# Kernel tuning notes

Hardware: AMD Instinct MI355X
Metric: run time of the kernel (lower is better)

## Reference

```python
import jax, jax.numpy as jnp
import numpy as np

# RRFU config (matches init_kwargs)
S = 2          # scale_factor
G = 4          # groups
K = 3          # sample_k
C = 64         # in_channels
B, H, W_IN = 4, 128, 128
SC = S * S     # s_c
KC = K * K     # sample_c (3x3 = 9)


def setup_inputs() -> dict:
    key = jax.random.key(0)
    ks = jax.random.split(key, 9)
    x = jax.random.normal(ks[0], (B, C, H, W_IN), jnp.float32)
    # 1x1 conv weights stored as (out_ch, in_ch); std chosen per module's init
    # (mask convs are zero-init in the original; use small random so math is nontrivial)
    w_off = jax.random.normal(ks[1], (G * SC * 2, C), jnp.float32) * 0.001
    b_off = jnp.zeros((G * SC * 2,), jnp.float32)
    w_offm = jax.random.normal(ks[2], (G * SC * 2, C), jnp.float32) * 0.01
    b_offm = jnp.zeros((G * SC * 2,), jnp.float32)
    w_sk = jax.random.normal(ks[3], (KC, C), jnp.float32) * 0.005
    b_sk = jnp.zeros((KC,), jnp.float32)
    w_km = jax.random.normal(ks[4], (KC, C), jnp.float32) * 0.01
    b_km = jnp.zeros((KC,), jnp.float32)
    return {"x": x, "w_off": w_off, "b_off": b_off, "w_offm": w_offm,
            "b_offm": b_offm, "w_sk": w_sk, "b_sk": b_sk, "w_km": w_km, "b_km": b_km}


def _conv1x1(x, w, b):
    return jnp.einsum('oc,bchw->bohw', w, x) + b[None, :, None, None]


def _bilinear_border(img, iy, ix):
    """img: (Cg,H,W); iy,ix: (Ho,Wo) pixel coords. grid_sample bilinear, padding_mode='border'."""
    Hh, Ww = img.shape[1], img.shape[2]
    ix = jnp.clip(ix, 0.0, Ww - 1.0)
    iy = jnp.clip(iy, 0.0, Hh - 1.0)
    x0 = jnp.floor(ix)
    y0 = jnp.floor(iy)
    wx = ix - x0
    wy = iy - y0
    x0i = x0.astype(jnp.int32)
    y0i = y0.astype(jnp.int32)
    x1i = jnp.minimum(x0i + 1, Ww - 1)
    y1i = jnp.minimum(y0i + 1, Hh - 1)
    v00 = img[:, y0i, x0i]
    v01 = img[:, y0i, x1i]
    v10 = img[:, y1i, x0i]
    v11 = img[:, y1i, x1i]
    return (v00 * (1 - wx) * (1 - wy) + v01 * wx * (1 - wy)
            + v10 * (1 - wx) * wy + v11 * wx * wy)


def reference(x, w_off, b_off, w_offm, b_offm, w_sk, b_sk, w_km, b_km):
    b0, c0, h0, w0 = x.shape
    # learned offsets, gated by sigmoid mask
    off = _conv1x1(x, w_off, b_off) * jax.nn.sigmoid(_conv1x1(x, w_offm, b_offm))
    bg = b0 * G
    # (b, g*S*S*2, h, w) -> (bg, S, S, 2, h, w) -> (bg, h, S, w, S, 2) -> (bg, S*h, S*w, 2)
    off = off.reshape(bg, S, S, 2, h0, w0).transpose(0, 4, 1, 5, 2, 3).reshape(bg, S * h0, S * w0, 2)
    Ho, Wo = S * h0, S * w0
    # coord_base + offset, normalized then un-normalized for align_corners=False grid_sample
    cx = jnp.arange(Wo, dtype=x.dtype) + 0.5
    cy = jnp.arange(Ho, dtype=x.dtype) + 0.5
    ix = (cx[None, None, :] + off[..., 0]) * (w0 / Wo) - 0.5  # (bg, Ho, Wo)
    iy = (cy[None, :, None] + off[..., 1]) * (h0 / Ho) - 0.5
    x_r = x.reshape(bg, c0 // G, h0, w0)
    x_def = jax.vmap(_bilinear_border)(x_r, iy, ix).reshape(b0, c0, Ho, Wo)
    # CARAFE-style dynamic reassembly: softmax kernel over 3x3 neighborhood
    sk = _conv1x1(x_def, w_sk, b_sk) * jax.nn.sigmoid(_conv1x1(x_def, w_km, b_km))
    skn = jax.nn.softmax(sk, axis=1)  # (b, 9, Ho, Wo)
    pad = K // 2
    xp = jnp.pad(x_def, ((0, 0), (0, 0), (pad, pad), (pad, pad)))  # zero pad like F.unfold
    out = jnp.zeros_like(x_def)
    for ky in range(K):  # fixed 3x3 taps; avoids materializing (b,c,9,Ho,Wo)
        for kx in range(K):
            out = out + skn[:, ky * K + kx][:, None] * xp[:, :, ky:ky + Ho, kx:kx + Wo]
    return out
```

## Files before the change

### kernel.cpp

```cpp
#include <hip/hip_runtime.h>
#include <hip/hip_fp16.h>

typedef _Float16 h2 __attribute__((ext_vector_type(2)));

constexpr int Bc  = 4;
constexpr int Cc  = 64;
constexpr int H0  = 128;
constexpr int W0  = 128;
constexpr int HW  = H0 * W0;
constexpr int Gc  = 4;
constexpr int HOc = H0 * 2;
constexpr int WOc = W0 * 2;

constexpr int TW = 16;
constexpr int TH = 8;
constexpr int HX = TW + 2;
constexpr int HY = TH + 2;
constexpr int NHALO = HX * HY;
constexpr int NTASK = Gc * NHALO;

constexpr int SXC = 10;
constexpr int SYC = 6;
constexpr int SN  = SXC * SYC;
constexpr int NPAIR = Cc / 2;

__device__ __forceinline__ float dot2(h2 a, unsigned bw, float c) {
    union { unsigned u; h2 h; } cv; cv.u = bw;
#if __has_builtin(__builtin_amdgcn_fdot2)
    return __builtin_amdgcn_fdot2(a, cv.h, c, false);
#else
    return fmaf((float)a[0], (float)cv.h[0],
                fmaf((float)a[1], (float)cv.h[1], c));
#endif
}

__global__ __launch_bounds__(256) void kT_prep(
    const float* __restrict__ w_off, const float* __restrict__ w_offm,
    const float* __restrict__ w_sk,  const float* __restrict__ w_km,
    float* __restrict__ wT, __half2* __restrict__ wpk)
{
    const int i = blockIdx.x * 256 + threadIdx.x;
    if (i < 4096) {
        const int mat = i >> 11;
        const int rem = i & 2047;
        const int c   = rem >> 5;
        const int r   = rem & 31;
        wT[i] = (mat ? w_offm : w_off)[r * Cc + c];
    } else if (i < 4096 + 576) {
        const int j   = i - 4096;
        const int mat = j >= 288;
        const int jj  = mat ? j - 288 : j;
        const int k   = jj >> 5;
        const int c2  = jj & 31;
        const float* src = mat ? w_km : w_sk;
        wpk[j] = __floats2half2_rn(src[k * Cc + 2 * c2],
                                   src[k * Cc + 2 * c2 + 1]);
    }
}

__global__ __launch_bounds__(256) void k0_offsets(
    const float* __restrict__ x, const float* __restrict__ wT,
    const float* __restrict__ b_off, const float* __restrict__ b_offm,
    __half2* __restrict__ offbuf)
{
    const int b    = blockIdx.y;
    const int t    = threadIdx.x;
    const int wave = t >> 6, lane = t & 63;
    const int r0   = __builtin_amdgcn_readfirstlane((wave & 1) * 16);
    const int px   = blockIdx.x * 128 + (wave >> 1) * 64 + lane;

    float a[16], m[16];
#pragma unroll
    for (int q = 0; q < 16; ++q) { a[q] = 0.f; m[q] = 0.f; }

    const float* xp  = x + (size_t)b * Cc * HW + px;
    const float* w0p = wT + r0;
    const float* w1p = wT + 2048 + r0;

#pragma unroll 2
    for (int c = 0; c < Cc; ++c) {
        const float xv = xp[c * HW];
#pragma unroll
        for (int q = 0; q < 16; ++q) {
            a[q] = fmaf(w0p[c * 32 + q], xv, a[q]);
            m[q] = fmaf(w1p[c * 32 + q], xv, m[q]);
        }
    }

#pragma unroll
    for (int j = 0; j < 8; ++j) {
        const int r = r0 + 2 * j;
        const float sx = 1.f / (1.f + __expf(-(m[2 * j]     + b_offm[r])));
        const float sy = 1.f / (1.f + __expf(-(m[2 * j + 1] + b_offm[r + 1])));
        const float vx = (a[2 * j]     + b_off[r])     * sx;
        const float vy = (a[2 * j + 1] + b_off[r + 1]) * sy;
        offbuf[((size_t)b * 16 + (r >> 1)) * HW + px] = __floats2half2_rn(vx, vy);
    }
}

__global__ __launch_bounds__(256) void k1_fused(
    const float* __restrict__ x, const __half2* __restrict__ offbuf,
    const unsigned* __restrict__ wsku, const float* __restrict__ b_sk,
    const float* __restrict__ b_km,
    float* __restrict__ out)
{
    __shared__ h2    xd2[NPAIR][NHALO];
    __shared__ float ovl[2304];
    h2*       xstage2 = (h2*)ovl;
    float*    kmb     = ovl;
    unsigned* sknb    = (unsigned*)(ovl + 128 * 9);

    const unsigned* wkmu = wsku + 288;

    const int b    = blockIdx.y;
    const int tile = blockIdx.x;
    const int ox = (tile & 15) * TW;
    const int oy = (tile >> 4) * TH;
    const int t  = threadIdx.x;
    const int syr = (oy >> 1) - 1;
    const int sxr = (ox >> 1) - 1;

    const float* xb = x + (size_t)b * Cc * HW;

    for (int i = t; i < NPAIR * SN; i += 256) {
        const int c2  = i / SN;
        const int rem = i - c2 * SN;
        const int r   = rem / SXC;
        const int j   = rem - r * SXC;
        const int yy  = min(max(syr + r, 0), H0 - 1);
        const int xx  = min(max(sxr + j, 0), W0 - 1);
        const float f0 = xb[(size_t)(2 * c2)     * HW + yy * W0 + xx];
        const float f1 = xb[(size_t)(2 * c2 + 1) * HW + yy * W0 + xx];
        xstage2[i] = h2{(_Float16)f0, (_Float16)f1};
    }
    __syncthreads();

    for (int task = t; task < NTASK; task += 256) {
        const int g   = task / NHALO;
        const int pix = task - g * NHALO;
        const int hy  = pix / HX;
        const int hx  = pix - hy * HX;
        const int gy  = oy - 1 + hy;
        const int gx  = ox - 1 + hx;
        if (gy < 0 || gy >= HOc || gx < 0 || gx >= WOc) {
#pragma unroll
            for (int p = 0; p < 8; ++p) xd2[g * 8 + p][pix] = (h2)0;
            continue;
        }
        const int sy = gy & 1, sx = gx & 1;
        const int h  = gy >> 1, w  = gx >> 1;
        const __half2 o2 = offbuf[((size_t)b * 16 + g * 4 + sy * 2 + sx) * HW
                                  + h * W0 + w];
        const float offx = __low2float(o2);
        const float offy = __high2float(o2);

        float ix = ((float)gx + 0.5f + offx) * 0.5f - 0.5f;
        float iy = ((float)gy + 0.5f + offy) * 0.5f - 0.5f;
        ix = fminf(fmaxf(ix, 0.f), (float)(W0 - 1));
        iy = fminf(fmaxf(iy, 0.f), (float)(H0 - 1));
        const float x0f = floorf(ix), y0f = floorf(iy);
        const float wx = ix - x0f,   wy = iy - y0f;
        const int x0 = (int)x0f, y0 = (int)y0f;
        const int x1 = min(x0 + 1, W0 - 1), y1 = min(y0 + 1, H0 - 1);
        const float w00 = (1.f - wx) * (1.f - wy);
        const float w01 = wx * (1.f - wy);
        const float w10 = (1.f - wx) * wy;
        const float w11 = wx * wy;

        const int j0 = x0 - sxr, j1 = x1 - sxr;
        const int i0 = y0 - syr, i1 = y1 - syr;
        const bool inl = (j0 >= 0) & (j1 < SXC) & (i0 >= 0) & (i1 < SYC);

        if (inl) {
            const int o00 = i0 * SXC + j0, o01 = i0 * SXC + j1;
            const int o10 = i1 * SXC + j0, o11 = i1 * SXC + j1;
            const _Float16 W00 = (_Float16)w00, W01 = (_Float16)w01;
            const _Float16 W10 = (_Float16)w10, W11 = (_Float16)w11;
            const h2* s2 = xstage2 + (g * 8) * SN;
#pragma unroll
            for (int p = 0; p < 8; ++p) {
                const h2* pc = s2 + p * SN;
                xd2[g * 8 + p][pix] =
                    pc[o00] * W00 + pc[o01] * W01 + pc[o10] * W10 + pc[o11] * W11;
            }
        } else {
            const int o00 = y0 * W0 + x0, o01 = y0 * W0 + x1;
            const int o10 = y1 * W0 + x0, o11 = y1 * W0 + x1;
#pragma unroll
            for (int p = 0; p < 8; ++p) {
                const float* pc0 = xb + (size_t)(g * 16 + 2 * p) * HW;
                const float* pc1 = pc0 + HW;
                const float v0 = w00 * pc0[o00] + w01 * pc0[o01]
                               + w10 * pc0[o10] + w11 * pc0[o11];
                const float v1 = w00 * pc1[o00] + w01 * pc1[o01]
                               + w10 * pc1[o10] + w11 * pc1[o11];
                xd2[g * 8 + p][pix] = h2{(_Float16)v0, (_Float16)v1};
            }
        }
    }
    __syncthreads();

    {
        const int p   = t & 127;
        const int ctr = ((p >> 4) + 1) * HX + (p & 15) + 1;
        h2 xv[NPAIR];
#pragma unroll
        for (int c2 = 0; c2 < NPAIR; ++c2) xv[c2] = xd2[c2][ctr];

        float acc[9];
        if (t < 128) {
#pragma unroll
            for (int k = 0; k < 9; ++k) {
                float a = 0.f;
#pragma unroll
                for (int c2 = 0; c2 < NPAIR; ++c2)
                    a = dot2(xv[c2], wsku[k * 32 + c2], a);
                acc[k] = a;
            }
        } else {
#pragma unroll
            for (int k = 0; k < 9; ++k) {
                float a = 0.f;
#pragma unroll
                for (int c2 = 0; c2 < NPAIR; ++c2)
                    a = dot2(xv[c2], wkmu[k * 32 + c2], a);
                kmb[p * 9 + k] = a;
            }
        }
        __syncthreads();

        if (t < 128) {
            float sv[9], mx = -1e30f;
#pragma unroll
            for (int k = 0; k < 9; ++k) {
                const float z = kmb[p * 9 + k] + b_km[k];
                sv[k] = (acc[k] + b_sk[k]) / (1.f + __expf(-z));
                mx = fmaxf(mx, sv[k]);
            }
            float sum = 0.f;
#pragma unroll
            for (int k = 0; k < 9; ++k) { sv[k] = __expf(sv[k] - mx); sum += sv[k]; }
            const float inv = 1.f / sum;
#pragma unroll
            for (int k = 0; k < 9; ++k) {
                const unsigned hu = __half_as_ushort(__float2half(sv[k] * inv));
                sknb[p * 9 + k] = hu | (hu << 16);
            }
        }
    }
    __syncthreads();

    {
        const int sq    = t & 31;
        const int chunk = t >> 5;
        const int sqx = sq & 7, sqy = sq >> 3;
        const int hx0 = 2 * sqx, hy0 = 2 * sqy;
        const int p00 = (2 * sqy) * TW + 2 * sqx;

        union { unsigned u; h2 h; } s00[9], s01[9], s10[9], s11[9];
#pragma unroll
        for (int k = 0; k < 9; ++k) {
            s00[k].u = sknb[p00 * 9 + k];        s01[k].u = sknb[(p00 + 1) * 9 + k];
            s10[k].u = sknb[(p00 + TW) * 9 + k]; s11[k].u = sknb[(p00 + TW + 1) * 9 + k];
        }
        const int orow0 = oy + 2 * sqy, ocol0 = ox + 2 * sqx;

#pragma unroll
        for (int i = 0; i < 4; ++i) {
            const int pr = chunk * 4 + i;
            h2 wd[4][4];
#pragma unroll
            for (int ry = 0; ry < 4; ++ry) {
                const int base = (hy0 + ry) * HX + hx0;
#pragma unroll
                for (int rx = 0; rx < 4; ++rx)
                    wd[ry][rx] = xd2[pr][base + rx];
            }
            h2 a00 = (h2)0, a01 = (h2)0, a10 = (h2)0, a11 = (h2)0;
#pragma unroll
            for (int ky = 0; ky < 3; ++ky)
#pragma unroll
                for (int kx = 0; kx < 3; ++kx) {
                    const int k = ky * 3 + kx;
                    a00 += s00[k].h * wd[ky    ][kx    ];
                    a01 += s01[k].h * wd[ky    ][kx + 1];
                    a10 += s10[k].h * wd[ky + 1][kx    ];
                    a11 += s11[k].h * wd[ky + 1][kx + 1];
                }
            float* ob0 = out + ((size_t)(b * Cc + 2 * pr)) * (HOc * WOc)
                             + (size_t)orow0 * WOc + ocol0;
            float* ob1 = ob0 + (size_t)(HOc * WOc);
            *reinterpret_cast<float2*>(ob0)       = make_float2((float)a00[0], (float)a01[0]);
            *reinterpret_cast<float2*>(ob0 + WOc) = make_float2((float)a10[0], (float)a11[0]);
            *reinterpret_cast<float2*>(ob1)       = make_float2((float)a00[1], (float)a01[1]);
            *reinterpret_cast<float2*>(ob1 + WOc) = make_float2((float)a10[1], (float)a11[1]);
        }
    }
}

extern "C" void kernel_launch(void* const* d_in, const int* in_sizes, int n_in,
                              void* d_out, int out_size, void* d_ws, size_t ws_size,
                              hipStream_t stream)
{
    const float* x      = (const float*)d_in[0];
    const float* w_off  = (const float*)d_in[1];
    const float* b_off  = (const float*)d_in[2];
    const float* w_offm = (const float*)d_in[3];
    const float* b_offm = (const float*)d_in[4];
    const float* w_sk   = (const float*)d_in[5];
    const float* b_sk   = (const float*)d_in[6];
    const float* w_km   = (const float*)d_in[7];
    const float* b_km   = (const float*)d_in[8];
    float* outp = (float*)d_out;

    const size_t off_bytes = (size_t)Bc * 16 * HW * sizeof(__half2);
    const size_t wt_bytes  = 4096 * sizeof(float);
    const size_t pk_bytes  = 576 * sizeof(__half2);
    if (ws_size < off_bytes + wt_bytes + pk_bytes) return;
    __half2* offbuf = (__half2*)d_ws;
    float*   wT     = (float*)((char*)d_ws + off_bytes);
    __half2* wpk    = (__half2*)((char*)d_ws + off_bytes + wt_bytes);

    dim3 blk(256);
    hipLaunchKernelGGL(kT_prep, dim3(19), blk, 0, stream,
                       w_off, w_offm, w_sk, w_km, wT, wpk);

    dim3 g0(HW / 128, Bc);
    hipLaunchKernelGGL(k0_offsets, g0, blk, 0, stream,
                       x, wT, b_off, b_offm, offbuf);

    dim3 g1(512, Bc);
    hipLaunchKernelGGL(k1_fused, g1, blk, 0, stream,
                       x, offbuf, (const unsigned*)wpk, b_sk, b_km, outp);
}
```

Before: 68.26 us.

## Emit channel-last fp16 copy of x and pixel-major offsets for fused kernel

```diff
diff --git a/kernel.cpp b/kernel.cpp
--- a/kernel.cpp
+++ b/kernel.cpp
@@ -24,8 +24,10 @@
 constexpr int SN  = SXC * SYC;
 constexpr int NPAIR = Cc / 2;
 
+union hu32 { unsigned u; h2 h; };
+
 __device__ __forceinline__ float dot2(h2 a, unsigned bw, float c) {
-    union { unsigned u; h2 h; } cv; cv.u = bw;
+    hu32 cv; cv.u = bw;
 #if __has_builtin(__builtin_amdgcn_fdot2)
     return __builtin_amdgcn_fdot2(a, cv.h, c, false);
 #else
@@ -37,17 +39,19 @@
 __global__ __launch_bounds__(256) void kT_prep(
     const float* __restrict__ w_off, const float* __restrict__ w_offm,
     const float* __restrict__ w_sk,  const float* __restrict__ w_km,
-    float* __restrict__ wT, __half2* __restrict__ wpk)
+    __half2* __restrict__ wpk0, __half2* __restrict__ wpk)
 {
     const int i = blockIdx.x * 256 + threadIdx.x;
-    if (i < 4096) {
-        const int mat = i >> 11;
-        const int rem = i & 2047;
-        const int c   = rem >> 5;
+    if (i < 2048) {
+        const int c2  = i >> 6;
+        const int rem = i & 63;
+        const int mat = rem >> 5;
         const int r   = rem & 31;
-        wT[i] = (mat ? w_offm : w_off)[r * Cc + c];
-    } else if (i < 4096 + 576) {
-        const int j   = i - 4096;
+        const float* src = mat ? w_offm : w_off;
+        wpk0[i] = __floats2half2_rn(src[r * Cc + 2 * c2],
+                                    src[r * Cc + 2 * c2 + 1]);
+    } else if (i < 2048 + 576) {
+        const int j   = i - 2048;
         const int mat = j >= 288;
         const int jj  = mat ? j - 288 : j;
         const int k   = jj >> 5;
@@ -59,47 +63,57 @@
 }
 
 __global__ __launch_bounds__(256) void k0_offsets(
-    const float* __restrict__ x, const float* __restrict__ wT,
+    const float* __restrict__ x, const unsigned* __restrict__ wpk0,
     const float* __restrict__ b_off, const float* __restrict__ b_offm,
-    __half2* __restrict__ offbuf)
+    __half2* __restrict__ offbuf, unsigned* __restrict__ xt)
 {
     const int b    = blockIdx.y;
     const int t    = threadIdx.x;
     const int wave = t >> 6, lane = t & 63;
-    const int r0   = __builtin_amdgcn_readfirstlane((wave & 1) * 16);
-    const int px   = blockIdx.x * 128 + (wave >> 1) * 64 + lane;
-
-    float a[16], m[16];
-#pragma unroll
-    for (int q = 0; q < 16; ++q) { a[q] = 0.f; m[q] = 0.f; }
-
-    const float* xp  = x + (size_t)b * Cc * HW + px;
-    const float* w0p = wT + r0;
-    const float* w1p = wT + 2048 + r0;
-
-#pragma unroll 2
-    for (int c = 0; c < Cc; ++c) {
-        const float xv = xp[c * HW];
-#pragma unroll
-        for (int q = 0; q < 16; ++q) {
-            a[q] = fmaf(w0p[c * 32 + q], xv, a[q]);
-            m[q] = fmaf(w1p[c * 32 + q], xv, m[q]);
-        }
-    }
-
-#pragma unroll
-    for (int j = 0; j < 8; ++j) {
+    const int r0   = __builtin_amdgcn_readfirstlane(wave * 8);
+    const int px   = blockIdx.x * 64 + lane;
+
+    float a[8], m[8];
+#pragma unroll
+    for (int q = 0; q < 8; ++q) { a[q] = 0.f; m[q] = 0.f; }
+    unsigned xtr[NPAIR];
+
+    const float*    xp = x + (size_t)b * Cc * HW + px;
+    const unsigned* wp = wpk0 + r0;
+
+#pragma unroll 4
+    for (int c2 = 0; c2 < NPAIR; ++c2) {
+        const float x0 = xp[(2 * c2)     * HW];
+        const float x1 = xp[(2 * c2 + 1) * HW];
+        hu32 xh; xh.h = h2{(_Float16)x0, (_Float16)x1};
+        xtr[c2] = xh.u;
+#pragma unroll
+        for (int q = 0; q < 8; ++q) {
+            a[q] = dot2(xh.h, wp[c2 * 64 + q],      a[q]);
+            m[q] = dot2(xh.h, wp[c2 * 64 + 32 + q], m[q]);
+        }
+    }
+
+    __half2* ob = offbuf + ((size_t)b * HW + px) * 16 + (r0 >> 1);
+#pragma unroll
+    for (int j = 0; j < 4; ++j) {
         const int r = r0 + 2 * j;
         const float sx = 1.f / (1.f + __expf(-(m[2 * j]     + b_offm[r])));
         const float sy = 1.f / (1.f + __expf(-(m[2 * j + 1] + b_offm[r + 1])));
         const float vx = (a[2 * j]     + b_off[r])     * sx;
         const float vy = (a[2 * j + 1] + b_off[r + 1]) * sy;
-        offbuf[((size_t)b * 16 + (r >> 1)) * HW + px] = __floats2half2_rn(vx, vy);
+        ob[j] = __floats2half2_rn(vx, vy);
+    }
+
+    if (wave == 0) {
+        unsigned* xo = xt + ((size_t)b * HW + px) * NPAIR;
+#pragma unroll
+        for (int c2 = 0; c2 < NPAIR; ++c2) xo[c2] = xtr[c2];
     }
 }
 
 __global__ __launch_bounds__(256) void k1_fused(
-    const float* __restrict__ x, const __half2* __restrict__ offbuf,
+    const unsigned* __restrict__ xt, const __half2* __restrict__ offbuf,
     const unsigned* __restrict__ wsku, const float* __restrict__ b_sk,
     const float* __restrict__ b_km,
     float* __restrict__ out)
@@ -120,18 +134,18 @@
     const int syr = (oy >> 1) - 1;
     const int sxr = (ox >> 1) - 1;
 
-    const float* xb = x + (size_t)b * Cc * HW;
-
+    const unsigned* xtb = xt + (size_t)b * HW * NPAIR;
+    const __half2*  obb = offbuf + (size_t)b * HW * 16;
+
+    unsigned* xs_u = (unsigned*)xstage2;
     for (int i = t; i < NPAIR * SN; i += 256) {
-        const int c2  = i / SN;
-        const int rem = i - c2 * SN;
-        const int r   = rem / SXC;
-        const int j   = rem - r * SXC;
+        const int c2  = i & 31;
+        const int pos = i >> 5;
+        const int r   = pos / SXC;
+        const int j   = pos - r * SXC;
         const int yy  = min(max(syr + r, 0), H0 - 1);
         const int xx  = min(max(sxr + j, 0), W0 - 1);
-        const float f0 = xb[(size_t)(2 * c2)     * HW + yy * W0 + xx];
-        const float f1 = xb[(size_t)(2 * c2 + 1) * HW + yy * W0 + xx];
-        xstage2[i] = h2{(_Float16)f0, (_Float16)f1};
+        xs_u[c2 * SN + pos] = xtb[(yy * W0 + xx) * NPAIR + c2];
     }
     __syncthreads();
 
@@ -149,8 +163,7 @@
         }
         const int sy = gy & 1, sx = gx & 1;
         const int h  = gy >> 1, w  = gx >> 1;
-        const __half2 o2 = offbuf[((size_t)b * 16 + g * 4 + sy * 2 + sx) * HW
-                                  + h * W0 + w];
+        const __half2 o2 = obb[(size_t)(h * W0 + w) * 16 + g * 4 + sy * 2 + sx];
         const float offx = __low2float(o2);
         const float offy = __high2float(o2);
 
@@ -171,11 +184,12 @@
         const int i0 = y0 - syr, i1 = y1 - syr;
         const bool inl = (j0 >= 0) & (j1 < SXC) & (i0 >= 0) & (i1 < SYC);
 
+        const _Float16 W00 = (_Float16)w00, W01 = (_Float16)w01;
+        const _Float16 W10 = (_Float16)w10, W11 = (_Float16)w11;
+
         if (inl) {
             const int o00 = i0 * SXC + j0, o01 = i0 * SXC + j1;
             const int o10 = i1 * SXC + j0, o11 = i1 * SXC + j1;
-            const _Float16 W00 = (_Float16)w00, W01 = (_Float16)w01;
-            const _Float16 W10 = (_Float16)w10, W11 = (_Float16)w11;
             const h2* s2 = xstage2 + (g * 8) * SN;
 #pragma unroll
             for (int p = 0; p < 8; ++p) {
@@ -184,17 +198,16 @@
                     pc[o00] * W00 + pc[o01] * W01 + pc[o10] * W10 + pc[o11] * W11;
             }
         } else {
-            const int o00 = y0 * W0 + x0, o01 = y0 * W0 + x1;
-            const int o10 = y1 * W0 + x0, o11 = y1 * W0 + x1;
+            const int o00 = (y0 * W0 + x0) * NPAIR, o01 = (y0 * W0 + x1) * NPAIR;
+            const int o10 = (y1 * W0 + x0) * NPAIR, o11 = (y1 * W0 + x1) * NPAIR;
 #pragma unroll
             for (int p = 0; p < 8; ++p) {
-                const float* pc0 = xb + (size_t)(g * 16 + 2 * p) * HW;
-                const float* pc1 = pc0 + HW;
-                const float v0 = w00 * pc0[o00] + w01 * pc0[o01]
-                               + w10 * pc0[o10] + w11 * pc0[o11];
-                const float v1 = w00 * pc1[o00] + w01 * pc1[o01]
-                               + w10 * pc1[o10] + w11 * pc1[o11];
-                xd2[g * 8 + p][pix] = h2{(_Float16)v0, (_Float16)v1};
+                const int c2 = g * 8 + p;
+                hu32 v00, v01, v10, v11;
+                v00.u = xtb[o00 + c2]; v01.u = xtb[o01 + c2];
+                v10.u = xtb[o10 + c2]; v11.u = xtb[o11 + c2];
+                xd2[c2][pix] =
+                    v00.h * W00 + v01.h * W01 + v10.h * W10 + v11.h * W11;
             }
         }
     }
@@ -257,7 +270,7 @@
         const int hx0 = 2 * sqx, hy0 = 2 * sqy;
         const int p00 = (2 * sqy) * TW + 2 * sqx;
 
-        union { unsigned u; h2 h; } s00[9], s01[9], s10[9], s11[9];
+        hu32 s00[9], s01[9], s10[9], s11[9];
 #pragma unroll
         for (int k = 0; k < 9; ++k) {
             s00[k].u = sknb[p00 * 9 + k];        s01[k].u = sknb[(p00 + 1) * 9 + k];
@@ -313,23 +326,25 @@
     const float* b_km   = (const float*)d_in[8];
     float* outp = (float*)d_out;
 
-    const size_t off_bytes = (size_t)Bc * 16 * HW * sizeof(__half2);
-    const size_t wt_bytes  = 4096 * sizeof(float);
-    const size_t pk_bytes  = 576 * sizeof(__half2);
-    if (ws_size < off_bytes + wt_bytes + pk_bytes) return;
-    __half2* offbuf = (__half2*)d_ws;
-    float*   wT     = (float*)((char*)d_ws + off_bytes);
-    __half2* wpk    = (__half2*)((char*)d_ws + off_bytes + wt_bytes);
+    const size_t off_bytes  = (size_t)Bc * HW * 16 * sizeof(__half2);
+    const size_t xt_bytes   = (size_t)Bc * HW * NPAIR * sizeof(unsigned);
+    const size_t wpk0_bytes = 2048 * sizeof(__half2);
+    const size_t wpk_bytes  = 576 * sizeof(__half2);
+    if (ws_size < off_bytes + xt_bytes + wpk0_bytes + wpk_bytes) return;
+    __half2*  offbuf = (__half2*)d_ws;
+    unsigned* xtbuf  = (unsigned*)((char*)d_ws + off_bytes);
+    __half2*  wpk0   = (__half2*)((char*)d_ws + off_bytes + xt_bytes);
+    __half2*  wpk    = (__half2*)((char*)d_ws + off_bytes + xt_bytes + wpk0_bytes);
 
     dim3 blk(256);
-    hipLaunchKernelGGL(kT_prep, dim3(19), blk, 0, stream,
-                       w_off, w_offm, w_sk, w_km, wT, wpk);
-
-    dim3 g0(HW / 128, Bc);
+    hipLaunchKernelGGL(kT_prep, dim3(11), blk, 0, stream,
+                       w_off, w_offm, w_sk, w_km, wpk0, wpk);
+
+    dim3 g0(HW / 64, Bc);
     hipLaunchKernelGGL(k0_offsets, g0, blk, 0, stream,
-                       x, wT, b_off, b_offm, offbuf);
+                       x, (const unsigned*)wpk0, b_off, b_offm, offbuf, xtbuf);
 
     dim3 g1(512, Bc);
     hipLaunchKernelGGL(k1_fused, g1, blk, 0, stream,
-                       x, offbuf, (const unsigned*)wpk, b_sk, b_km, outp);
-}
+                       xtbuf, offbuf, (const unsigned*)wpk, b_sk, b_km, outp);
+}
```

New measurement: 60.71 us. 11.1% less time.
